# Kernel optimization log

Measured on AMD Instinct MI355X. Metric: run time of the kernel, lower is better.

## Reference

```python
import jax, jax.numpy as jnp
import numpy as np

CUTOFF = [2000, 10000, 50000]
INPUT_DIM = 1024
PROJECT_DIMS = [256, 64]  # input_dim / 4, input_dim / 16


def gelu(x):
    # exact erf-based GELU, as in the source
    return x * 0.5 * (1.0 + jax.lax.erf(x / jnp.sqrt(2.0).astype(x.dtype)))


def _ce(logits, labels):
    # sparse softmax cross entropy per row
    lp = jax.nn.log_softmax(logits, axis=-1)
    return -jnp.take_along_axis(lp, labels[:, None], axis=1)[:, 0]


def setup_inputs() -> dict:
    key = jax.random.key(0)
    ks = jax.random.split(key, 10)
    N = 4096
    head_dim = CUTOFF[0] + (len(CUTOFF) - 1)  # 2002
    s = 0.02
    inp = {
        "inputs": jax.random.normal(ks[0], (N, INPUT_DIM), jnp.float32),
        "labels": jax.random.randint(ks[1], (N,), 0, CUTOFF[-1], jnp.int64),
        "head_proj": jax.random.normal(ks[2], (INPUT_DIM, INPUT_DIM), jnp.float32) * s,
        "head_w": jax.random.normal(ks[3], (INPUT_DIM, head_dim), jnp.float32) * s,
        "head_b": jnp.zeros((head_dim,), jnp.float32),
        "tail1_proj_w": jax.random.normal(ks[4], (INPUT_DIM, PROJECT_DIMS[0]), jnp.float32) * s,
        "tail1_w": jax.random.normal(ks[5], (PROJECT_DIMS[0], CUTOFF[1] - CUTOFF[0]), jnp.float32) * s,
        "tail1_b": jnp.zeros((CUTOFF[1] - CUTOFF[0],), jnp.float32),
        "tail2_proj_w": jax.random.normal(ks[6], (INPUT_DIM, PROJECT_DIMS[1]), jnp.float32) * s,
        "tail2_w": jax.random.normal(ks[7], (PROJECT_DIMS[1], CUTOFF[2] - CUTOFF[1]), jnp.float32) * s,
        "tail2_b": jnp.zeros((CUTOFF[2] - CUTOFF[1],), jnp.float32),
    }
    return inp


def reference(inputs, labels, head_proj, head_w, head_b,
              tail1_proj_w, tail1_w, tail1_b,
              tail2_proj_w, tail2_w, tail2_b):
    # Adaptive softmax negative log-likelihood, per token ([N]).
    # Instead of boolean_mask gather / SparseTensor scatter (dynamic shapes),
    # compute per-cluster CE densely and mask — identical math where mask holds.
    tails = [(tail1_proj_w, tail1_w, tail1_b), (tail2_proj_w, tail2_w, tail2_b)]
    head_labels = labels
    loss = jnp.zeros(labels.shape, jnp.float32)
    for i, (pw, w, b) in enumerate(tails):
        lo, hi = CUTOFF[i], CUTOFF[i + 1]
        mask = (labels >= lo) & (labels < hi)
        head_labels = jnp.where(mask, CUTOFF[0] + i, head_labels)
        tail_logits = gelu(inputs @ pw) @ w + b  # [N, hi-lo]
        tail_lab = jnp.clip(labels - lo, 0, hi - lo - 1)
        loss = loss + jnp.where(mask, _ce(tail_logits, tail_lab), 0.0)
    head_logits = gelu(inputs @ head_proj) @ head_w + head_b  # [N, cutoff0+2]
    loss = loss + _ce(head_logits, head_labels)
    return loss
```

## Files before the change

### kernel.cpp

```cpp
#include <hip/hip_runtime.h>
#include <hip/hip_bf16.h>
#include <math.h>

#define NTOK 4096
#define DIM  1024

typedef __attribute__((ext_vector_type(8))) short short8;
typedef __attribute__((ext_vector_type(4))) float f32x4;

__device__ __forceinline__ short f2bf(float f) {
    return __builtin_bit_cast(short, __float2bfloat16(f));
}
__device__ __forceinline__ float bf2f(short s) {
    unsigned u = ((unsigned)(unsigned short)s) << 16;
    return __builtin_bit_cast(float, u);
}
__device__ __forceinline__ float gelu_exact(float x) {
    return x * 0.5f * (1.0f + erff(x * 0.70710678118654752f));
}

__device__ __forceinline__
void transpose_tile(const float* __restrict__ src, short* __restrict__ dst,
                    int K, int V, int Vpad, int vt, int kt)
{
    __shared__ float tile[32][33];
    const int v0 = vt * 32, k0 = kt * 32;
    const int tx = threadIdx.x & 31, ty = threadIdx.x >> 5;
    #pragma unroll
    for (int i = 0; i < 4; ++i) {
        const int k = k0 + ty + 8 * i, v = v0 + tx;
        tile[ty + 8 * i][tx] = (k < K && v < V) ? src[(size_t)k * V + v] : 0.f;
    }
    __syncthreads();
    #pragma unroll
    for (int i = 0; i < 4; ++i) {
        const int v = v0 + ty + 8 * i, k = k0 + tx;
        if (v < Vpad && k < K) dst[(size_t)v * K + k] = f2bf(tile[tx][ty + 8 * i]);
    }
}

__global__ __launch_bounds__(256)
void prep_kernel(const float* __restrict__ X, short* __restrict__ Xb,
                 const float* __restrict__ hp,  short* __restrict__ WhpT,
                 const float* __restrict__ t1p, short* __restrict__ W1pT,
                 const float* __restrict__ t2p, short* __restrict__ W2pT,
                 const float* __restrict__ hw,  short* __restrict__ WhT,
                 const float* __restrict__ t1w, short* __restrict__ W1T,
                 const float* __restrict__ t2w, short* __restrict__ W2T,
                 const int* __restrict__ labels,
                 int* __restrict__ idx1, int* __restrict__ idx2,
                 int* __restrict__ counts)
{
    int b = blockIdx.x;
    if (b < 2048) {
        const size_t idx = ((size_t)b * 256 + threadIdx.x) * 8;
        const float4 a = *reinterpret_cast<const float4*>(X + idx);
        const float4 c = *reinterpret_cast<const float4*>(X + idx + 4);
        short8 v;
        v[0] = f2bf(a.x); v[1] = f2bf(a.y); v[2] = f2bf(a.z); v[3] = f2bf(a.w);
        v[4] = f2bf(c.x); v[5] = f2bf(c.y); v[6] = f2bf(c.z); v[7] = f2bf(c.w);
        *reinterpret_cast<short8*>(Xb + idx) = v;
        return;
    }
    b -= 2048;
    if (b < 1024) { transpose_tile(hp,  WhpT, 1024, 1024,  1024,  b % 32,   b / 32);   return; }
    b -= 1024;
    if (b < 256)  { transpose_tile(t1p, W1pT, 1024, 256,   256,   b % 8,    b / 8);    return; }
    b -= 256;
    if (b < 64)   { transpose_tile(t2p, W2pT, 1024, 64,    64,    b % 2,    b / 2);    return; }
    b -= 64;
    if (b < 2048) { transpose_tile(hw,  WhT,  1024, 2002,  2048,  b % 64,   b / 64);   return; }
    b -= 2048;
    if (b < 2048) { transpose_tile(t1w, W1T,  256,  8000,  8192,  b % 256,  b / 256);  return; }
    b -= 2048;
    if (b < 2560) { transpose_tile(t2w, W2T,  64,  40000,  40960, b % 1280, b / 1280); return; }
    b -= 2560;
    {
        const int i = b * 256 + threadIdx.x;
        const int lab = labels[i];
        if (lab >= 2000 && lab < 10000) idx1[atomicAdd(&counts[0], 1)] = i;
        else if (lab >= 10000)          idx2[atomicAdd(&counts[1], 1)] = i;
    }
}

__global__ __launch_bounds__(512, 2)
void proj5(const short* __restrict__ Xb,
           const short* __restrict__ WhpT, const short* __restrict__ W1pT,
           const short* __restrict__ W2pT,
           short* __restrict__ H, short* __restrict__ T1, short* __restrict__ T2)
{
    constexpr int KSTEP = 256, CHB = 32 * KSTEP * 2;
    __shared__ char sA[2][CHB];
    const int tid = threadIdx.x, w = tid >> 6, l = tid & 63;
    const int arow = l & 15, kg = l >> 4;
    const int c_g = (blockIdx.y * 8 + w) * 16;
    const short* Bt; short* Pout; int Vout, cl; bool active = true;
    if (c_g < 1024)      { Bt = WhpT; Pout = H;  Vout = 1024; cl = c_g; }
    else if (c_g < 1280) { Bt = W1pT; Pout = T1; Vout = 256;  cl = c_g - 1024; }
    else if (c_g < 1344) { Bt = W2pT; Pout = T2; Vout = 64;   cl = c_g - 1280; }
    else                 { Bt = W2pT; Pout = T2; Vout = 64;   cl = 0; active = false; }

    short8 breg[32];
    const short* bp = Bt + (size_t)(cl + arow) * DIM + kg * 8;
    #pragma unroll
    for (int f = 0; f < 32; ++f) breg[f] = *reinterpret_cast<const short8*>(bp + f * 32);

    const int g0 = blockIdx.x * 128;
    short8 st8[2];
    auto load_chunk = [&](int rt, int kh) {
        #pragma unroll
        for (int j = 0; j < 2; ++j) {
            const int v = tid + j * 512;
            const int m = v >> 5, c8 = v & 31;
            st8[j] = *reinterpret_cast<const short8*>(
                Xb + (size_t)(g0 + rt * 32 + m) * DIM + kh * KSTEP + c8 * 8);
        }
    };
    auto store_chunk = [&](int buf) {
        char* base = &sA[buf][0];
        #pragma unroll
        for (int j = 0; j < 2; ++j) {
            const int v = tid + j * 512;
            const int m = v >> 5, c8 = v & 31;
            *reinterpret_cast<short8*>(
                base + (((m * KSTEP + c8 * 8) * 2) ^ ((m & 7) << 4))) = st8[j];
        }
    };

    load_chunk(0, 0); store_chunk(0); __syncthreads();
    f32x4 acc[2] = {(f32x4){0.f,0.f,0.f,0.f}, (f32x4){0.f,0.f,0.f,0.f}};
    for (int rt = 0; rt < 4; ++rt) {
        #pragma unroll
        for (int kh = 0; kh < 4; ++kh) {
            const int buf = kh & 1;
            const bool last = (rt == 3) && (kh == 3);
            if (!last) load_chunk(kh < 3 ? rt : rt + 1, (kh + 1) & 3);
            const char* base = &sA[buf][0];
            #pragma unroll
            for (int f = 0; f < 8; ++f) {
                const short8 af0 = *reinterpret_cast<const short8*>(
                    base + (((arow * KSTEP + f * 32 + kg * 8) * 2) ^ ((arow & 7) << 4)));
                const short8 af1 = *reinterpret_cast<const short8*>(
                    base + ((((16 + arow) * KSTEP + f * 32 + kg * 8) * 2) ^ ((arow & 7) << 4)));
                acc[0] = __builtin_amdgcn_mfma_f32_16x16x32_bf16(af0, breg[kh * 8 + f], acc[0], 0, 0, 0);
                acc[1] = __builtin_amdgcn_mfma_f32_16x16x32_bf16(af1, breg[kh * 8 + f], acc[1], 0, 0, 0);
            }
            if (kh == 3) {
                if (active) {
                    #pragma unroll
                    for (int mr = 0; mr < 2; ++mr)
                        #pragma unroll
                        for (int r = 0; r < 4; ++r)
                            Pout[(size_t)(g0 + rt * 32 + mr * 16 + kg * 4 + r) * Vout + cl + arow] =
                                f2bf(gelu_exact(acc[mr][r]));
                }
                acc[0] = (f32x4){0.f,0.f,0.f,0.f};
                acc[1] = (f32x4){0.f,0.f,0.f,0.f};
            }
            if (!last) store_chunk(buf ^ 1);
            __syncthreads();
        }
    }
}

template<int K, int NT, bool IDENT, int RPG>
__device__ __forceinline__
void ce_core(const short* __restrict__ A, const short* __restrict__ Bt,
             const float* __restrict__ bias, const int* __restrict__ rows,
             const int* __restrict__ countp, float* __restrict__ sum_acc,
             int V, int bx, int by,
             char* __restrict__ sA, float* __restrict__ lsum, int* __restrict__ rlds)
{
    constexpr int KSTEP = (K > 256) ? 256 : K;
    constexpr int NKH   = K / KSTEP;
    constexpr int NKFS  = KSTEP / 32;
    constexpr int NKF   = K / 32;
    constexpr int CHB   = 32 * KSTEP * 2;
    constexpr int NV8   = 32 * KSTEP / 8;
    constexpr int VPT   = (NV8 + 511) / 512;

    const int cnt = IDENT ? NTOK : *countp;
    const int g0 = bx * RPG;
    if (g0 >= cnt) return;
    const int ng = min(RPG, cnt - g0);
    const int tid = threadIdx.x;
    const int w = tid >> 6, l = tid & 63;
    const int arow = l & 15, kg = l >> 4;

    for (int t = tid; t < RPG; t += 512) {
        lsum[t] = 0.f;
        rlds[t] = IDENT ? (g0 + t) : rows[min(g0 + t, cnt - 1)];
    }

    int ct[NT]; float cb[NT]; short8 breg[NT][NKF];
    #pragma unroll
    for (int t = 0; t < NT; ++t) {
        ct[t] = (by * 8 + w) * (16 * NT) + t * 16;
        const int col = ct[t] + arow;
        cb[t] = (col < V) ? __expf(bias[col]) : 0.f;
        const short* bp = Bt + (size_t)(ct[t] + arow) * K + kg * 8;
        #pragma unroll
        for (int f = 0; f < NKF; ++f)
            breg[t][f] = *reinterpret_cast<const short8*>(bp + f * 32);
    }
    __syncthreads();

    const int NRT = (ng + 31) / 32;

    short8 st8[VPT];
    auto load_chunk = [&](int c) {
        const int rt = c / NKH, kh = c % NKH, rb = rt * 32;
        #pragma unroll
        for (int j = 0; j < VPT; ++j) {
            const int v = tid + j * 512;
            if (v < NV8) {
                const int m = v / (KSTEP / 8), c8 = v % (KSTEP / 8);
                st8[j] = *reinterpret_cast<const short8*>(
                    A + (size_t)rlds[min(rb + m, RPG - 1)] * K + kh * KSTEP + c8 * 8);
            }
        }
    };
    auto store_chunk = [&](int buf) {
        char* base = sA + buf * CHB;
        #pragma unroll
        for (int j = 0; j < VPT; ++j) {
            const int v = tid + j * 512;
            if (v < NV8) {
                const int m = v / (KSTEP / 8), c8 = v % (KSTEP / 8);
                *reinterpret_cast<short8*>(
                    base + (((m * KSTEP + c8 * 8) * 2) ^ ((m & 7) << 4))) = st8[j];
            }
        }
    };

    load_chunk(0); store_chunk(0); __syncthreads();

    f32x4 acc[2][NT];
    #pragma unroll
    for (int mr = 0; mr < 2; ++mr)
        #pragma unroll
        for (int t = 0; t < NT; ++t) acc[mr][t] = (f32x4){0.f,0.f,0.f,0.f};

    for (int rt = 0; rt < NRT; ++rt) {
        #pragma unroll
        for (int kh = 0; kh < NKH; ++kh) {
            const int c   = rt * NKH + kh;
            const int buf = (NKH > 1) ? (kh & 1) : (rt & 1);
            const bool last = (c + 1 == NRT * NKH);
            if (!last) load_chunk(c + 1);
            const char* base = sA + buf * CHB;
            #pragma unroll
            for (int f = 0; f < NKFS; ++f) {
                const short8 af0 = *reinterpret_cast<const short8*>(
                    base + (((arow * KSTEP + f * 32 + kg * 8) * 2) ^ ((arow & 7) << 4)));
                const short8 af1 = *reinterpret_cast<const short8*>(
                    base + ((((16 + arow) * KSTEP + f * 32 + kg * 8) * 2) ^ ((arow & 7) << 4)));
                #pragma unroll
                for (int t = 0; t < NT; ++t) {
                    acc[0][t] = __builtin_amdgcn_mfma_f32_16x16x32_bf16(
                        af0, breg[t][kh * NKFS + f], acc[0][t], 0, 0, 0);
                    acc[1][t] = __builtin_amdgcn_mfma_f32_16x16x32_bf16(
                        af1, breg[t][kh * NKFS + f], acc[1][t], 0, 0, 0);
                }
            }
            if (kh == NKH - 1) {
                const int rb = rt * 32;
                #pragma unroll
                for (int mr = 0; mr < 2; ++mr) {
                    float sacc[4] = {0.f, 0.f, 0.f, 0.f};
                    #pragma unroll
                    for (int t = 0; t < NT; ++t)
                        #pragma unroll
                        for (int r = 0; r < 4; ++r)
                            sacc[r] = fmaf(__expf(acc[mr][t][r]), cb[t], sacc[r]);
                    #pragma unroll
                    for (int r = 0; r < 4; ++r) {
                        float v = sacc[r];
                        v += __shfl_xor(v, 1); v += __shfl_xor(v, 2);
                        v += __shfl_xor(v, 4); v += __shfl_xor(v, 8);
                        if (arow == 0) atomicAdd(&lsum[rb + mr * 16 + kg * 4 + r], v);
                    }
                    #pragma unroll
                    for (int t = 0; t < NT; ++t) acc[mr][t] = (f32x4){0.f,0.f,0.f,0.f};
                }
            }
            if (!last) store_chunk(buf ^ 1);
            __syncthreads();
        }
    }
    for (int t = tid; t < ng; t += 512)
        atomicAdd(&sum_acc[rlds[t]], lsum[t]);
}

__device__ __forceinline__
void ce_reg64(const short* __restrict__ A, const short* __restrict__ Bt,
              const float* __restrict__ bias, const int* __restrict__ rows,
              const int* __restrict__ countp, float* __restrict__ sum_acc,
              int V, int bx, int by,
              float* __restrict__ lsum, int* __restrict__ rlds)
{
    constexpr int NT = 4, RPG = 256;
    const int cnt = *countp;
    const int g0 = bx * RPG;
    if (g0 >= cnt) return;
    const int ng = min(RPG, cnt - g0);
    const int tid = threadIdx.x;
    const int w = tid >> 6, l = tid & 63;
    const int arow = l & 15, kg = l >> 4;

    for (int t = tid; t < RPG; t += 512) {
        lsum[t] = 0.f;
        rlds[t] = rows[min(g0 + t, cnt - 1)];
    }

    int ct[NT]; float cb[NT]; short8 breg[NT][2];
    #pragma unroll
    for (int t = 0; t < NT; ++t) {
        ct[t] = (by * 8 + w) * 64 + t * 16;
        const int col = ct[t] + arow;
        cb[t] = (col < V) ? __expf(bias[col]) : 0.f;
        const short* bp = Bt + (size_t)(ct[t] + arow) * 64 + kg * 8;
        breg[t][0] = *reinterpret_cast<const short8*>(bp);
        breg[t][1] = *reinterpret_cast<const short8*>(bp + 32);
    }
    __syncthreads();

    auto load_tile = [&](int rt, short8 (&dst)[2][2]) {
        #pragma unroll
        for (int mr = 0; mr < 2; ++mr) {
            const int r = rlds[rt * 32 + mr * 16 + arow];
            const short* ap = A + (size_t)r * 64 + kg * 8;
            dst[mr][0] = *reinterpret_cast<const short8*>(ap);
            dst[mr][1] = *reinterpret_cast<const short8*>(ap + 32);
        }
    };
    auto compute_tile = [&](int rt, const short8 (&Ar)[2][2]) {
        f32x4 acc[2][NT];
        #pragma unroll
        for (int mr = 0; mr < 2; ++mr)
            #pragma unroll
            for (int t = 0; t < NT; ++t) acc[mr][t] = (f32x4){0.f,0.f,0.f,0.f};
        #pragma unroll
        for (int f = 0; f < 2; ++f)
            #pragma unroll
            for (int mr = 0; mr < 2; ++mr)
                #pragma unroll
                for (int t = 0; t < NT; ++t)
                    acc[mr][t] = __builtin_amdgcn_mfma_f32_16x16x32_bf16(
                        Ar[mr][f], breg[t][f], acc[mr][t], 0, 0, 0);
        const int rb = rt * 32;
        #pragma unroll
        for (int mr = 0; mr < 2; ++mr) {
            float sacc[4] = {0.f, 0.f, 0.f, 0.f};
            #pragma unroll
            for (int t = 0; t < NT; ++t)
                #pragma unroll
                for (int r = 0; r < 4; ++r)
                    sacc[r] = fmaf(__expf(acc[mr][t][r]), cb[t], sacc[r]);
            #pragma unroll
            for (int r = 0; r < 4; ++r) {
                float v = sacc[r];
                v += __shfl_xor(v, 1); v += __shfl_xor(v, 2);
                v += __shfl_xor(v, 4); v += __shfl_xor(v, 8);
                if (arow == 0) atomicAdd(&lsum[rb + mr * 16 + kg * 4 + r], v);
            }
        }
    };

    short8 A0[2][2], A1[2][2];
    load_tile(0, A0);
    load_tile(1, A1);
    #pragma unroll
    for (int rt = 0; rt < 8; rt += 2) {
        compute_tile(rt, A0);
        if (rt + 2 < 8) load_tile(rt + 2, A0);
        compute_tile(rt + 1, A1);
        if (rt + 3 < 8) load_tile(rt + 3, A1);
    }

    __syncthreads();
    for (int t = tid; t < ng; t += 512)
        atomicAdd(&sum_acc[rlds[t]], lsum[t]);
}

__global__ __launch_bounds__(512, 2)
void ce_head(const short* __restrict__ H, const short* __restrict__ WhT,
             const float* __restrict__ head_b, float* __restrict__ hsum)
{
    __shared__ char  sA[2][16384];
    __shared__ float lsum[128];
    __shared__ int   rlds[128];
    ce_core<1024, 1, true, 128>(H, WhT, head_b, nullptr, nullptr, hsum, 2002,
                                blockIdx.x, blockIdx.y, &sA[0][0], lsum, rlds);
}

#define NB_T2 1280
__global__ __launch_bounds__(512, 4)
void ce_tails(const short* __restrict__ T1, const short* __restrict__ W1T,
              const float* __restrict__ t1b,
              const short* __restrict__ T2, const short* __restrict__ W2T,
              const float* __restrict__ t2b,
              const int* __restrict__ idx1, const int* __restrict__ idx2,
              const int* __restrict__ counts, float* __restrict__ tsum)
{
    __shared__ char  sA[2][16384];
    __shared__ float lsum[256];
    __shared__ int   rlds[256];
    const int b = blockIdx.x;
    if (b < NB_T2) {
        ce_reg64(T2, W2T, t2b, idx2, &counts[1], tsum, 40000,
                 b / 80, b % 80, lsum, rlds);
    } else {
        const int b2 = b - NB_T2;
        ce_core<256, 2, false, 128>(T1, W1T, t1b, idx1, &counts[0], tsum, 8000,
                                    b2 / 32, b2 % 32, &sA[0][0], lsum, rlds);
    }
}

__global__ __launch_bounds__(256)
void finalize_kernel(const int* __restrict__ labels,
                     const short* __restrict__ H,  const short* __restrict__ WhT,
                     const float* __restrict__ head_b,
                     const short* __restrict__ T1, const short* __restrict__ W1T,
                     const float* __restrict__ t1b,
                     const short* __restrict__ T2, const short* __restrict__ W2T,
                     const float* __restrict__ t2b,
                     const float* __restrict__ hsum, const float* __restrict__ tsum,
                     float* __restrict__ out)
{
    const int r = blockIdx.x * 4 + (threadIdx.x >> 6);
    const int l = threadIdx.x & 63;
    if (r >= NTOK) return;
    const int lab = labels[r];
    int labH = lab;
    if (lab >= 10000) labH = 2001; else if (lab >= 2000) labH = 2000;

    float d = 0.f;
    {
        const short* a = H   + (size_t)r    * 1024 + l * 16;
        const short* b = WhT + (size_t)labH * 1024 + l * 16;
        #pragma unroll
        for (int u = 0; u < 2; ++u) {
            const short8 av = *reinterpret_cast<const short8*>(a + u * 8);
            const short8 bv = *reinterpret_cast<const short8*>(b + u * 8);
            #pragma unroll
            for (int e = 0; e < 8; ++e) d = fmaf(bf2f(av[e]), bf2f(bv[e]), d);
        }
    }
    float td = 0.f;
    if (lab >= 2000) {
        const short* a; const short* b; int nl;
        if (lab < 10000) { a = T1 + (size_t)r * 256; b = W1T + (size_t)(lab - 2000) * 256; nl = 32; }
        else             { a = T2 + (size_t)r * 64;  b = W2T + (size_t)(lab - 10000) * 64; nl = 8; }
        if (l < nl) {
            const short8 av = *reinterpret_cast<const short8*>(a + l * 8);
            const short8 bv = *reinterpret_cast<const short8*>(b + l * 8);
            #pragma unroll
            for (int e = 0; e < 8; ++e) td = fmaf(bf2f(av[e]), bf2f(bv[e]), td);
        }
    }
    #pragma unroll
    for (int off = 32; off; off >>= 1) { d += __shfl_xor(d, off); td += __shfl_xor(td, off); }
    if (l == 0) {
        float loss = logf(hsum[r]) - (d + head_b[labH]);
        if (lab >= 2000) {
            const float tb = (lab < 10000) ? t1b[lab - 2000] : t2b[lab - 10000];
            loss += logf(tsum[r]) - (td + tb);
        }
        out[r] = loss;
    }
}

extern "C" void kernel_launch(void* const* d_in, const int* in_sizes, int n_in,
                              void* d_out, int out_size, void* d_ws, size_t ws_size,
                              hipStream_t stream) {
    (void)in_sizes; (void)n_in; (void)out_size; (void)ws_size;
    const float* X         = (const float*)d_in[0];
    const int*   labels    = (const int*)  d_in[1];
    const float* head_proj = (const float*)d_in[2];
    const float* head_w    = (const float*)d_in[3];
    const float* head_b    = (const float*)d_in[4];
    const float* t1p       = (const float*)d_in[5];
    const float* t1w       = (const float*)d_in[6];
    const float* t1b       = (const float*)d_in[7];
    const float* t2p       = (const float*)d_in[8];
    const float* t2w       = (const float*)d_in[9];
    const float* t2b       = (const float*)d_in[10];
    float* out = (float*)d_out;

    char* ws = (char*)d_ws;
    int*   counts = (int*)ws;
    int*   idx1   = (int*)(ws + 1024);
    int*   idx2   = (int*)(ws + 1024 + 16384);
    float* hsum   = (float*)(ws + 65536);
    float* tsum   = hsum + NTOK;

    short* p = (short*)(ws + 131072);
    short* Xb   = p; p += (size_t)NTOK * 1024;
    short* WhpT = p; p += (size_t)1024 * 1024;
    short* W1pT = p; p += (size_t)256  * 1024;
    short* W2pT = p; p += (size_t)64   * 1024;
    short* WhT  = p; p += (size_t)2048 * 1024;
    short* W1T  = p; p += (size_t)8192 * 256;
    short* W2T  = p; p += (size_t)40960 * 64;
    short* H    = p; p += (size_t)NTOK * 1024;
    short* T1   = p; p += (size_t)NTOK * 256;
    short* T2   = p; p += (size_t)NTOK * 64;

    hipMemsetAsync(counts, 0, 16, stream);
    hipMemsetAsync(hsum, 0, 2 * NTOK * sizeof(float), stream);

    prep_kernel<<<10064, 256, 0, stream>>>(X, Xb, head_proj, WhpT, t1p, W1pT,
                                           t2p, W2pT, head_w, WhT, t1w, W1T, t2w, W2T,
                                           labels, idx1, idx2, counts);
    proj5<<<dim3(32, 11), 512, 0, stream>>>(Xb, WhpT, W1pT, W2pT, H, T1, T2);

    ce_head<<<dim3(32, 16), 512, 0, stream>>>(H, WhT, head_b, hsum);
    ce_tails<<<NB_T2 + 256, 512, 0, stream>>>(T1, W1T, t1b, T2, W2T, t2b,
                                              idx1, idx2, counts, tsum);

    finalize_kernel<<<NTOK / 4, 256, 0, stream>>>(
        labels, H, WhT, head_b, T1, W1T, t1b, T2, W2T, t2b, hsum, tsum, out);
}
```

Baseline: 185.6 us.

## Fuse head and tail CE kernels into one launch with register-resident head B tiles

Replaces the separate ce_head and ce_tails launches with a single ce_fused kernel whose block ranges dispatch to tail2, a new head path, and tail1, sharing one LDS buffer. The new head path keeps each wave's 16 output columns of the head weight in registers, double-buffered across K chunks, and streams token tiles through swizzled LDS, computing exp-sum partials per 32-row tile. This is meant to remove a launch boundary, let head and tail work overlap across CUs, and cut LDS traffic for the weight operand. In exchange, head blocks now run under a 4-blocks-per-SM launch bound with heavier register use, there is a sync per K chunk, and per-block work changes.

Result: slower. 192.0 us (+3.4%).

```diff
diff --git a/kernel.cpp b/kernel.cpp
--- a/kernel.cpp
+++ b/kernel.cpp
@@ -293,6 +293,106 @@
 }
 
 __device__ __forceinline__
+void ce_head2(const short* __restrict__ A, const short* __restrict__ Bt,
+              const float* __restrict__ bias, float* __restrict__ sum_acc,
+              int bx, int by, char* __restrict__ sA, float* __restrict__ lsum)
+{
+    constexpr int K = 1024, KSTEP = 256, NKFS = 8;
+    constexpr int CHB = 32 * KSTEP * 2;
+    const int tid = threadIdx.x, w = tid >> 6, l = tid & 63;
+    const int arow = l & 15, kg = l >> 4;
+    const int g0 = bx * 128;
+
+    for (int t = tid; t < 128; t += 512) lsum[t] = 0.f;
+
+    const int ct  = (by * 8 + w) * 16;
+    const int col = ct + arow;
+    const float cb = (col < 2002) ? __expf(bias[col]) : 0.f;
+    const short* bbase = Bt + (size_t)col * K + kg * 8;
+
+    short8 b0[NKFS], b1[NKFS];
+    #pragma unroll
+    for (int f = 0; f < NKFS; ++f)
+        b0[f] = *reinterpret_cast<const short8*>(bbase + f * 32);
+
+    short8 st8[2];
+    auto load_chunk = [&](int c) {
+        const int rt = c >> 2, kh = c & 3;
+        #pragma unroll
+        for (int j = 0; j < 2; ++j) {
+            const int v = tid + j * 512;
+            const int m = v >> 5, c8 = v & 31;
+            st8[j] = *reinterpret_cast<const short8*>(
+                A + (size_t)(g0 + rt * 32 + m) * K + kh * KSTEP + c8 * 8);
+        }
+    };
+    auto store_chunk = [&](int buf) {
+        char* base = sA + buf * CHB;
+        #pragma unroll
+        for (int j = 0; j < 2; ++j) {
+            const int v = tid + j * 512;
+            const int m = v >> 5, c8 = v & 31;
+            *reinterpret_cast<short8*>(
+                base + (((m * KSTEP + c8 * 8) * 2) ^ ((m & 7) << 4))) = st8[j];
+        }
+    };
+    auto do_chunk = [&](const short8 (&bc)[NKFS], short8 (&bn)[NKFS],
+                        int rt, int kh, f32x4& a0, f32x4& a1) {
+        const int c = rt * 4 + kh;
+        const bool last = (c == 15);
+        if (!last) {
+            load_chunk(c + 1);
+            const int nkh = (kh + 1) & 3;
+            #pragma unroll
+            for (int f = 0; f < NKFS; ++f)
+                bn[f] = *reinterpret_cast<const short8*>(bbase + nkh * KSTEP + f * 32);
+        }
+        const char* base = sA + (kh & 1) * CHB;
+        #pragma unroll
+        for (int f = 0; f < NKFS; ++f) {
+            const short8 af0 = *reinterpret_cast<const short8*>(
+                base + (((arow * KSTEP + f * 32 + kg * 8) * 2) ^ ((arow & 7) << 4)));
+            const short8 af1 = *reinterpret_cast<const short8*>(
+                base + ((((16 + arow) * KSTEP + f * 32 + kg * 8) * 2) ^ ((arow & 7) << 4)));
+            a0 = __builtin_amdgcn_mfma_f32_16x16x32_bf16(af0, bc[f], a0, 0, 0, 0);
+            a1 = __builtin_amdgcn_mfma_f32_16x16x32_bf16(af1, bc[f], a1, 0, 0, 0);
+        }
+        if (kh == 3) {
+            const int rb = rt * 32;
+            #pragma unroll
+            for (int mr = 0; mr < 2; ++mr) {
+                f32x4& aa = (mr == 0) ? a0 : a1;
+                float sacc[4];
+                #pragma unroll
+                for (int r = 0; r < 4; ++r) sacc[r] = __expf(aa[r]) * cb;
+                #pragma unroll
+                for (int r = 0; r < 4; ++r) {
+                    float v = sacc[r];
+                    v += __shfl_xor(v, 1); v += __shfl_xor(v, 2);
+                    v += __shfl_xor(v, 4); v += __shfl_xor(v, 8);
+                    if (arow == 0) atomicAdd(&lsum[rb + mr * 16 + kg * 4 + r], v);
+                }
+            }
+            a0 = (f32x4){0.f,0.f,0.f,0.f};
+            a1 = (f32x4){0.f,0.f,0.f,0.f};
+        }
+        if (!last) store_chunk((kh & 1) ^ 1);
+        __syncthreads();
+    };
+
+    load_chunk(0); store_chunk(0); __syncthreads();
+    f32x4 a0 = {0.f,0.f,0.f,0.f}, a1 = {0.f,0.f,0.f,0.f};
+    for (int rt = 0; rt < 4; ++rt) {
+        do_chunk(b0, b1, rt, 0, a0, a1);
+        do_chunk(b1, b0, rt, 1, a0, a1);
+        do_chunk(b0, b1, rt, 2, a0, a1);
+        do_chunk(b1, b0, rt, 3, a0, a1);
+    }
+    for (int t = tid; t < 128; t += 512)
+        atomicAdd(&sum_acc[g0 + t], lsum[t]);
+}
+
+__device__ __forceinline__
 void ce_reg64(const short* __restrict__ A, const short* __restrict__ Bt,
               const float* __restrict__ bias, const int* __restrict__ rows,
               const int* __restrict__ countp, float* __restrict__ sum_acc,
@@ -383,37 +483,30 @@
         atomicAdd(&sum_acc[rlds[t]], lsum[t]);
 }
 
-__global__ __launch_bounds__(512, 2)
-void ce_head(const short* __restrict__ H, const short* __restrict__ WhT,
-             const float* __restrict__ head_b, float* __restrict__ hsum)
-{
-    __shared__ char  sA[2][16384];
-    __shared__ float lsum[128];
-    __shared__ int   rlds[128];
-    ce_core<1024, 1, true, 128>(H, WhT, head_b, nullptr, nullptr, hsum, 2002,
-                                blockIdx.x, blockIdx.y, &sA[0][0], lsum, rlds);
-}
-
-#define NB_T2 1280
 __global__ __launch_bounds__(512, 4)
-void ce_tails(const short* __restrict__ T1, const short* __restrict__ W1T,
+void ce_fused(const short* __restrict__ H,  const short* __restrict__ WhT,
+              const float* __restrict__ head_b, float* __restrict__ hsum,
+              const short* __restrict__ T1, const short* __restrict__ W1T,
               const float* __restrict__ t1b,
               const short* __restrict__ T2, const short* __restrict__ W2T,
               const float* __restrict__ t2b,
               const int* __restrict__ idx1, const int* __restrict__ idx2,
               const int* __restrict__ counts, float* __restrict__ tsum)
 {
-    __shared__ char  sA[2][16384];
-    __shared__ float lsum[256];
-    __shared__ int   rlds[256];
+    __shared__ char smem[33792];
     const int b = blockIdx.x;
-    if (b < NB_T2) {
+    if (b < 1280) {
         ce_reg64(T2, W2T, t2b, idx2, &counts[1], tsum, 40000,
-                 b / 80, b % 80, lsum, rlds);
+                 b / 80, b % 80, (float*)smem, (int*)(smem + 1024));
+    } else if (b < 1792) {
+        const int b2 = b - 1280;
+        ce_head2(H, WhT, head_b, hsum, b2 & 31, b2 >> 5,
+                 smem, (float*)(smem + 32768));
     } else {
-        const int b2 = b - NB_T2;
+        const int b3 = b - 1792;
         ce_core<256, 2, false, 128>(T1, W1T, t1b, idx1, &counts[0], tsum, 8000,
-                                    b2 / 32, b2 % 32, &sA[0][0], lsum, rlds);
+                                    b3 / 32, b3 % 32, smem,
+                                    (float*)(smem + 32768), (int*)(smem + 33280));
     }
 }
 
@@ -515,9 +608,9 @@
                                            labels, idx1, idx2, counts);
     proj5<<<dim3(32, 11), 512, 0, stream>>>(Xb, WhpT, W1pT, W2pT, H, T1, T2);
 
-    ce_head<<<dim3(32, 16), 512, 0, stream>>>(H, WhT, head_b, hsum);
-    ce_tails<<<NB_T2 + 256, 512, 0, stream>>>(T1, W1T, t1b, T2, W2T, t2b,
-                                              idx1, idx2, counts, tsum);
+    ce_fused<<<2048, 512, 0, stream>>>(H, WhT, head_b, hsum,
+                                       T1, W1T, t1b, T2, W2T, t2b,
+                                       idx1, idx2, counts, tsum);
 
     finalize_kernel<<<NTOK / 4, 256, 0, stream>>>(
         labels, H, WhT, head_b, T1, W1T, t1b, T2, W2T, t2b, hsum, tsum, out);
```
